# Kernel optimization log

Hardware: AMD Instinct MI355X
Metric: run time of the kernel (lower is better)

Reference implementation:

```python
import jax, jax.numpy as jnp
import numpy as np

LN_EPS = 1e-5
SUM_EPS = 1e-6
Q_EPS = 1e-8

def layernorm(x):
    # parameter-free LayerNorm over last axis (elementwise_affine=False)
    mu = jnp.mean(x, axis=-1, keepdims=True)
    var = jnp.mean(jnp.square(x - mu), axis=-1, keepdims=True)
    return (x - mu) * jax.lax.rsqrt(var + LN_EPS)

def ternary_quant(W):
    # BitNet-b1.58-style ternary quantization: scale = mean(|W|), Wq in {-1,0,1}*scale
    scale = jnp.mean(jnp.abs(W))
    Wq = jnp.clip(jnp.round(W / (scale + Q_EPS)), -1.0, 1.0) * scale
    return Wq

def setup_inputs() -> dict:
    key = jax.random.key(0)
    ks = jax.random.split(key, 8)
    B, S, F = 8, 2048, 2048
    x = jax.random.normal(ks[0], (B, S, F), dtype=jnp.float32)
    seq_pos_code = jnp.arange(S, dtype=jnp.int32)
    feature_pos_code = jnp.arange(F, dtype=jnp.int32)
    # TernaryMLP(F, F, residual=False): ternary-quantized linear F -> F
    W_v = jax.random.normal(ks[1], (F, F), dtype=jnp.float32) * (1.0 / np.sqrt(F))
    b_v = jnp.zeros((F,), dtype=jnp.float32)
    # left attn: Linear(F, 1)
    w_left = jax.random.normal(ks[2], (F, 1), dtype=jnp.float32) * (1.0 / np.sqrt(F))
    b_left = jnp.zeros((1,), dtype=jnp.float32)
    # right attn: Linear(S, 1)
    w_right = jax.random.normal(ks[3], (S, 1), dtype=jnp.float32) * (1.0 / np.sqrt(S))
    b_right = jnp.zeros((1,), dtype=jnp.float32)
    alpha = jax.random.uniform(ks[4], (1,), dtype=jnp.float32)
    return {"x": x, "seq_pos_code": seq_pos_code, "feature_pos_code": feature_pos_code,
            "W_v": W_v, "b_v": b_v, "w_left": w_left, "b_left": b_left,
            "w_right": w_right, "b_right": b_right, "alpha": alpha}

def reference(x, seq_pos_code, feature_pos_code, W_v, b_v, w_left, b_left, w_right, b_right, alpha):
    B, S, F = x.shape
    # value path: ternary-quantized linear (TernaryMLP, residual=False)
    Wq = ternary_quant(W_v)
    v = jnp.einsum('bsf,fg->bsg', x, Wq) + b_v  # [B,S,F]
    # left attention: Linear(F->1) -> [B,S,1]; transpose; LN over S; ReLU; transpose back
    la = (jnp.einsum('bsf,fo->bso', x, w_left) + b_left)[..., 0]  # [B,S]
    la = jax.nn.relu(layernorm(la))[..., None]                    # [B,S,1]
    la = la / (jnp.sum(la, axis=-1, keepdims=True) + SUM_EPS)     # normalize over last dim (size 1)
    # right attention: transpose -> [B,F,S]; Linear(S->1); transpose -> [B,1,F]; LN over F; ReLU
    ra = (jnp.einsum('bsf,so->bfo', x, w_right) + b_right)[..., 0]  # [B,F]
    ra = jax.nn.relu(layernorm(ra))[:, None, :]                     # [B,1,F]
    ra = ra / (jnp.sum(ra, axis=-1, keepdims=True) + SUM_EPS)       # normalize over F
    a = alpha[0]
    return (1.0 - a) * x + a * la * v * ra
```

## Files before the change

kernel.cpp:

```cpp
#include <hip/hip_runtime.h>
#include <hip/hip_bf16.h>
#include <stdint.h>

#define B_ 8
#define S_ 2048
#define F_ 2048
#define M_ (B_*S_)
#define K_ F_
#define N_ F_

typedef __attribute__((ext_vector_type(4))) float f32x4;
typedef __attribute__((ext_vector_type(8))) short short8;

__device__ __forceinline__ unsigned short f2bf(float f){
  unsigned u = __float_as_uint(f);
  u += 0x7FFFu + ((u >> 16) & 1u);
  return (unsigned short)(u >> 16);
}

__device__ __forceinline__ void gload16(const void* g, const void* l){
  __builtin_amdgcn_global_load_lds(
      (const __attribute__((address_space(1))) void*)g,
      (__attribute__((address_space(3))) void*)l,
      16, 0, 0);
}

__device__ __forceinline__ float waveReduce(float v){
  #pragma unroll
  for (int off = 32; off; off >>= 1) v += __shfl_down(v, off, 64);
  return v;
}

__device__ __forceinline__ float blockReduceAll(float v, float* sbuf){
  v = waveReduce(v);
  int lane = threadIdx.x & 63, w = threadIdx.x >> 6;
  __syncthreads();
  if (lane == 0) sbuf[w] = v;
  __syncthreads();
  return sbuf[0] + sbuf[1] + sbuf[2] + sbuf[3];
}

__global__ __launch_bounds__(256) void k_abs1(const float* __restrict__ W, float* __restrict__ part){
  __shared__ float sb[4];
  size_t idx = ((size_t)blockIdx.x * 256 + threadIdx.x) * 4;
  f32x4 v = *(const f32x4*)(W + idx);
  float s = fabsf(v[0]) + fabsf(v[1]) + fabsf(v[2]) + fabsf(v[3]);
  s = blockReduceAll(s, sb);
  if (threadIdx.x == 0) part[blockIdx.x] = s;
}

__global__ __launch_bounds__(256) void k_abs2(const float* __restrict__ part, float* __restrict__ scalep){
  __shared__ float sb[4];
  float s = 0.f;
  int t = threadIdx.x;
  #pragma unroll
  for (int i = 0; i < 16; i++) s += part[t + i*256];
  s = blockReduceAll(s, sb);
  if (t == 0) scalep[0] = s * (1.0f / ((float)F_ * (float)F_));
}

__global__ __launch_bounds__(256) void k_quantT(const float* __restrict__ W, unsigned short* __restrict__ BT,
                                                const float* __restrict__ scalep){
  __shared__ float tile[32][33];
  int gx = blockIdx.x * 32;
  int fy = blockIdx.y * 32;
  int tx = threadIdx.x & 31, ty = threadIdx.x >> 5;
  float inv = 1.0f / (scalep[0] + 1e-8f);
  #pragma unroll
  for (int i = 0; i < 4; i++){
    int f = fy + ty + i*8;
    tile[ty + i*8][tx] = W[(size_t)f * F_ + gx + tx];
  }
  __syncthreads();
  #pragma unroll
  for (int i = 0; i < 4; i++){
    int g = gx + ty + i*8;
    float w = tile[tx][ty + i*8];
    float t = rintf(w * inv);
    t = fminf(1.0f, fmaxf(-1.0f, t));
    BT[(size_t)g * K_ + fy + tx] = f2bf(t);
  }
}

__global__ __launch_bounds__(256) void k_front(const float* __restrict__ X, const float* __restrict__ wl,
                                               const float* __restrict__ bl, const float* __restrict__ wrt,
                                               unsigned short* __restrict__ XH, float* __restrict__ la_raw,
                                               float* __restrict__ ra_raw){
  __shared__ float lap[4][32];
  int t = threadIdx.x, w = t >> 6, lane = t & 63;
  int r0 = blockIdx.x * 32;
  int b  = r0 >> 11;
  int f0 = t * 8;
  f32x4 wl0 = *(const f32x4*)(wl + f0);
  f32x4 wl1 = *(const f32x4*)(wl + f0 + 4);
  float racc[8];
  #pragma unroll
  for (int j = 0; j < 8; j++) racc[j] = 0.f;

  for (int rr = 0; rr < 32; ++rr){
    int row = r0 + rr;
    const float* xr = X + (size_t)row * F_ + f0;
    f32x4 v0 = *(const f32x4*)(xr);
    f32x4 v1 = *(const f32x4*)(xr + 4);
    ushort4 p0, p1;
    p0.x = f2bf(v0[0]); p0.y = f2bf(v0[1]); p0.z = f2bf(v0[2]); p0.w = f2bf(v0[3]);
    p1.x = f2bf(v1[0]); p1.y = f2bf(v1[1]); p1.z = f2bf(v1[2]); p1.w = f2bf(v1[3]);
    unsigned short* xh = XH + (size_t)row * F_ + f0;
    *(ushort4*)(xh)     = p0;
    *(ushort4*)(xh + 4) = p1;
    float dot = v0[0]*wl0[0] + v0[1]*wl0[1] + v0[2]*wl0[2] + v0[3]*wl0[3]
              + v1[0]*wl1[0] + v1[1]*wl1[1] + v1[2]*wl1[2] + v1[3]*wl1[3];
    dot = waveReduce(dot);
    if (lane == 0) lap[w][rr] = dot;
    float wsr = wrt[row & (S_-1)];
    racc[0] += v0[0]*wsr; racc[1] += v0[1]*wsr; racc[2] += v0[2]*wsr; racc[3] += v0[3]*wsr;
    racc[4] += v1[0]*wsr; racc[5] += v1[1]*wsr; racc[6] += v1[2]*wsr; racc[7] += v1[3]*wsr;
  }
  __syncthreads();
  if (t < 32)
    la_raw[r0 + t] = lap[0][t] + lap[1][t] + lap[2][t] + lap[3][t] + bl[0];
  float* rb = ra_raw + b * F_ + f0;
  #pragma unroll
  for (int j = 0; j < 8; j++) atomicAdd(&rb[j], racc[j]);
}

__global__ __launch_bounds__(256) void k_ln_la(const float* __restrict__ la_raw, float* __restrict__ la){
  __shared__ float sb[4];
  int b = blockIdx.x;
  const float* p = la_raw + b * S_;
  int t = threadIdx.x;
  float v[8]; float s = 0.f, s2 = 0.f;
  #pragma unroll
  for (int i = 0; i < 8; i++){ v[i] = p[t + i*256]; s += v[i]; s2 += v[i]*v[i]; }
  s  = blockReduceAll(s,  sb);
  s2 = blockReduceAll(s2, sb);
  float mu  = s * (1.0f / S_);
  float var = s2 * (1.0f / S_) - mu*mu;
  float rstd = 1.0f / sqrtf(var + 1e-5f);
  #pragma unroll
  for (int i = 0; i < 8; i++){
    float x = (v[i] - mu) * rstd;
    x = fmaxf(x, 0.0f);
    la[b * S_ + t + i*256] = x / (x + 1e-6f);
  }
}

__global__ __launch_bounds__(256) void k_ln_ra(const float* __restrict__ ra_raw, const float* __restrict__ br,
                                               float* __restrict__ ra){
  __shared__ float sb[4];
  int b = blockIdx.x;
  const float* p = ra_raw + b * F_;
  int t = threadIdx.x;
  float bb = br[0];
  float v[8]; float s = 0.f, s2 = 0.f;
  #pragma unroll
  for (int i = 0; i < 8; i++){ v[i] = p[t + i*256] + bb; s += v[i]; s2 += v[i]*v[i]; }
  s  = blockReduceAll(s,  sb);
  s2 = blockReduceAll(s2, sb);
  float mu  = s * (1.0f / F_);
  float var = s2 * (1.0f / F_) - mu*mu;
  float rstd = 1.0f / sqrtf(var + 1e-5f);
  float r[8]; float sr = 0.f;
  #pragma unroll
  for (int i = 0; i < 8; i++){ r[i] = fmaxf((v[i] - mu) * rstd, 0.0f); sr += r[i]; }
  sr = blockReduceAll(sr, sb);
  float invs = 1.0f / (sr + 1e-6f);
  #pragma unroll
  for (int i = 0; i < 8; i++) ra[b * F_ + t + i*256] = r[i] * invs;
}

__global__ __launch_bounds__(256) void k_gemm(
    const unsigned short* __restrict__ A, const unsigned short* __restrict__ BT,
    const float* __restrict__ X, const float* __restrict__ la, const float* __restrict__ ra,
    const float* __restrict__ bv, const float* __restrict__ alphap, const float* __restrict__ scalep,
    float* __restrict__ Out)
{
  __shared__ __align__(128) char lds[32768];
  const int NBX = N_ / 128;
  int tid = threadIdx.x;
  int bid = blockIdx.x;
  const int nwg = (M_/128) * (N_/128);
  int cpx = nwg >> 3;
  int swz = (bid & 7) * cpx + (bid >> 3);
  int brow = swz / NBX, bcol = swz % NBX;
  int row0 = brow * 128, col0 = bcol * 128;

  int w = tid >> 6, lane = tid & 63;
  int wr = w >> 1, wc = w & 1;
  int lrow = lane & 15, kgrp = lane >> 4;

  f32x4 acc[4][4];
  #pragma unroll
  for (int m = 0; m < 4; m++)
    #pragma unroll
    for (int n = 0; n < 4; n++) acc[m][n] = (f32x4)(0.0f);

  int c0 = tid, c1 = tid + 256;
  int ar0 = c0 >> 2, ak0 = (((c0 & 3) ^ ((ar0 >> 1) & 3)) << 3);
  int ar1 = c1 >> 2, ak1 = (((c1 & 3) ^ ((ar1 >> 1) & 3)) << 3);
  const unsigned short* Ap0 = A  + (size_t)(row0 + ar0) * K_ + ak0;
  const unsigned short* Ap1 = A  + (size_t)(row0 + ar1) * K_ + ak1;
  const unsigned short* Bp0 = BT + (size_t)(col0 + ar0) * K_ + ak0;
  const unsigned short* Bp1 = BT + (size_t)(col0 + ar1) * K_ + ak1;
  int stoff = w * 1024;

  int aoff[4], boff[4];
  #pragma unroll
  for (int m = 0; m < 4; m++){
    int r  = wr*64 + m*16 + lrow;
    aoff[m] = r*64 + ((kgrp ^ ((r >> 1) & 3)) << 4);
    int rc = wc*64 + m*16 + lrow;
    boff[m] = 8192 + rc*64 + ((kgrp ^ ((rc >> 1) & 3)) << 4);
  }

  {
    char* base = lds;
    gload16(Ap0, base + stoff);
    gload16(Ap1, base + 4096 + stoff);
    gload16(Bp0, base + 8192 + stoff);
    gload16(Bp1, base + 12288 + stoff);
  }
  asm volatile("s_waitcnt vmcnt(0)" ::: "memory");
  __syncthreads();

  int cur = 0;
  for (int kt = 0; kt < K_/32; ++kt){
    if (kt < K_/32 - 1){
      char* nb = lds + (cur ^ 1) * 16384;
      const unsigned short* a0 = Ap0 + (kt+1)*32;
      const unsigned short* a1 = Ap1 + (kt+1)*32;
      const unsigned short* b0 = Bp0 + (kt+1)*32;
      const unsigned short* b1 = Bp1 + (kt+1)*32;
      gload16(a0, nb + stoff);
      gload16(a1, nb + 4096 + stoff);
      gload16(b0, nb + 8192 + stoff);
      gload16(b1, nb + 12288 + stoff);
    }
    const char* bb = lds + cur * 16384;
    short8 af[4], bfr[4];
    #pragma unroll
    for (int m = 0; m < 4; m++) af[m]  = *(const short8*)(bb + aoff[m]);
    #pragma unroll
    for (int n = 0; n < 4; n++) bfr[n] = *(const short8*)(bb + boff[n]);
    __builtin_amdgcn_s_setprio(1);
    #pragma unroll
    for (int m = 0; m < 4; m++)
      #pragma unroll
      for (int n = 0; n < 4; n++)
        acc[m][n] = __builtin_amdgcn_mfma_f32_16x16x32_bf16(af[m], bfr[n], acc[m][n], 0, 0, 0);
    __builtin_amdgcn_s_setprio(0);
    asm volatile("s_waitcnt vmcnt(0)" ::: "memory");
    __syncthreads();
    cur ^= 1;
  }

  float a = alphap[0];
  float scale = scalep[0];
  float oma = 1.0f - a;
  int bidx = row0 >> 11;
  const float* rab = ra + bidx * F_;
  #pragma unroll
  for (int m = 0; m < 4; m++){
    int rbase = row0 + wr*64 + m*16 + (lane >> 4) * 4;
    float lav[4];
    #pragma unroll
    for (int r = 0; r < 4; r++) lav[r] = la[rbase + r];
    #pragma unroll
    for (int n = 0; n < 4; n++){
      int col = col0 + wc*64 + n*16 + (lane & 15);
      float rav = rab[col];
      float bvv = bv[col];
      #pragma unroll
      for (int r = 0; r < 4; r++){
        int row = rbase + r;
        float v = acc[m][n][r] * scale + bvv;
        size_t idx = (size_t)row * N_ + col;
        Out[idx] = oma * X[idx] + a * lav[r] * v * rav;
      }
    }
  }
}

extern "C" void kernel_launch(void* const* d_in, const int* in_sizes, int n_in,
                              void* d_out, int out_size, void* d_ws, size_t ws_size,
                              hipStream_t stream){
  const float* x     = (const float*)d_in[0];
  const float* Wv    = (const float*)d_in[3];
  const float* bv    = (const float*)d_in[4];
  const float* wl    = (const float*)d_in[5];
  const float* bl    = (const float*)d_in[6];
  const float* wrt   = (const float*)d_in[7];
  const float* br    = (const float*)d_in[8];
  const float* alpha = (const float*)d_in[9];
  float* out = (float*)d_out;

  char* ws = (char*)d_ws;
  unsigned short* XH = (unsigned short*)(ws);
  unsigned short* BT = (unsigned short*)(ws + 67108864);
  float* la_raw = (float*)(ws + 75497472);
  float* la     = (float*)(ws + 75563008);
  float* ra_raw = (float*)(ws + 75628544);
  float* ra     = (float*)(ws + 75694080);
  float* part   = (float*)(ws + 75759616);
  float* scalep = (float*)(ws + 75776000);

  hipMemsetAsync(ra_raw, 0, B_ * F_ * sizeof(float), stream);
  k_abs1<<<4096, 256, 0, stream>>>(Wv, part);
  k_abs2<<<1, 256, 0, stream>>>(part, scalep);
  k_quantT<<<dim3(F_/32, F_/32), 256, 0, stream>>>(Wv, BT, scalep);
  k_front<<<M_/32, 256, 0, stream>>>(x, wl, bl, wrt, XH, la_raw, ra_raw);
  k_ln_la<<<B_, 256, 0, stream>>>(la_raw, la);
  k_ln_ra<<<B_, 256, 0, stream>>>(ra_raw, br, ra);
  k_gemm<<<2048, 256, 0, stream>>>(XH, BT, x, la, ra, bv, alpha, scalep, out);
}
```

Before: 527.0 us.

## Deepen GEMM LDS pipeline to four stages, merge LN kernels, unroll front loop

The GEMM main loop moves from a double-buffered LDS scheme with a full vmcnt(0) wait each step to a 4-stage ring buffer (64KB LDS), three tiles prefetched ahead and partial vmcnt waits. The aim is to hide global-to-LDS load latency behind the MFMA work. The two LayerNorm kernels become one 16-block launch, saving a launch. The front kernel processes two rows per iteration for more memory-level parallelism. The larger LDS footprint may lower occupancy per CU.

After: 465.8 us. -11.6%, faster.

```diff
diff --git a/kernel.cpp b/kernel.cpp
--- a/kernel.cpp
+++ b/kernel.cpp
@@ -97,24 +97,40 @@
   #pragma unroll
   for (int j = 0; j < 8; j++) racc[j] = 0.f;
 
-  for (int rr = 0; rr < 32; ++rr){
-    int row = r0 + rr;
-    const float* xr = X + (size_t)row * F_ + f0;
-    f32x4 v0 = *(const f32x4*)(xr);
-    f32x4 v1 = *(const f32x4*)(xr + 4);
-    ushort4 p0, p1;
-    p0.x = f2bf(v0[0]); p0.y = f2bf(v0[1]); p0.z = f2bf(v0[2]); p0.w = f2bf(v0[3]);
-    p1.x = f2bf(v1[0]); p1.y = f2bf(v1[1]); p1.z = f2bf(v1[2]); p1.w = f2bf(v1[3]);
-    unsigned short* xh = XH + (size_t)row * F_ + f0;
-    *(ushort4*)(xh)     = p0;
-    *(ushort4*)(xh + 4) = p1;
-    float dot = v0[0]*wl0[0] + v0[1]*wl0[1] + v0[2]*wl0[2] + v0[3]*wl0[3]
-              + v1[0]*wl1[0] + v1[1]*wl1[1] + v1[2]*wl1[2] + v1[3]*wl1[3];
-    dot = waveReduce(dot);
-    if (lane == 0) lap[w][rr] = dot;
-    float wsr = wrt[row & (S_-1)];
-    racc[0] += v0[0]*wsr; racc[1] += v0[1]*wsr; racc[2] += v0[2]*wsr; racc[3] += v0[3]*wsr;
-    racc[4] += v1[0]*wsr; racc[5] += v1[1]*wsr; racc[6] += v1[2]*wsr; racc[7] += v1[3]*wsr;
+  for (int rr = 0; rr < 32; rr += 2){
+    int rowA = r0 + rr, rowB = r0 + rr + 1;
+    const float* xrA = X + (size_t)rowA * F_ + f0;
+    const float* xrB = X + (size_t)rowB * F_ + f0;
+    f32x4 a0 = *(const f32x4*)(xrA);
+    f32x4 a1 = *(const f32x4*)(xrA + 4);
+    f32x4 b0 = *(const f32x4*)(xrB);
+    f32x4 b1 = *(const f32x4*)(xrB + 4);
+    ushort4 pa0, pa1, pb0, pb1;
+    pa0.x = f2bf(a0[0]); pa0.y = f2bf(a0[1]); pa0.z = f2bf(a0[2]); pa0.w = f2bf(a0[3]);
+    pa1.x = f2bf(a1[0]); pa1.y = f2bf(a1[1]); pa1.z = f2bf(a1[2]); pa1.w = f2bf(a1[3]);
+    pb0.x = f2bf(b0[0]); pb0.y = f2bf(b0[1]); pb0.z = f2bf(b0[2]); pb0.w = f2bf(b0[3]);
+    pb1.x = f2bf(b1[0]); pb1.y = f2bf(b1[1]); pb1.z = f2bf(b1[2]); pb1.w = f2bf(b1[3]);
+    unsigned short* xhA = XH + (size_t)rowA * F_ + f0;
+    unsigned short* xhB = XH + (size_t)rowB * F_ + f0;
+    *(ushort4*)(xhA)     = pa0;
+    *(ushort4*)(xhA + 4) = pa1;
+    *(ushort4*)(xhB)     = pb0;
+    *(ushort4*)(xhB + 4) = pb1;
+    float dotA = a0[0]*wl0[0] + a0[1]*wl0[1] + a0[2]*wl0[2] + a0[3]*wl0[3]
+               + a1[0]*wl1[0] + a1[1]*wl1[1] + a1[2]*wl1[2] + a1[3]*wl1[3];
+    float dotB = b0[0]*wl0[0] + b0[1]*wl0[1] + b0[2]*wl0[2] + b0[3]*wl0[3]
+               + b1[0]*wl1[0] + b1[1]*wl1[1] + b1[2]*wl1[2] + b1[3]*wl1[3];
+    #pragma unroll
+    for (int off = 32; off; off >>= 1){
+      dotA += __shfl_down(dotA, off, 64);
+      dotB += __shfl_down(dotB, off, 64);
+    }
+    if (lane == 0){ lap[w][rr] = dotA; lap[w][rr+1] = dotB; }
+    float wsA = wrt[rowA & (S_-1)], wsB = wrt[rowB & (S_-1)];
+    racc[0] += a0[0]*wsA + b0[0]*wsB; racc[1] += a0[1]*wsA + b0[1]*wsB;
+    racc[2] += a0[2]*wsA + b0[2]*wsB; racc[3] += a0[3]*wsA + b0[3]*wsB;
+    racc[4] += a1[0]*wsA + b1[0]*wsB; racc[5] += a1[1]*wsA + b1[1]*wsB;
+    racc[6] += a1[2]*wsA + b1[2]*wsB; racc[7] += a1[3]*wsA + b1[3]*wsB;
   }
   __syncthreads();
   if (t < 32)
@@ -124,49 +140,36 @@
   for (int j = 0; j < 8; j++) atomicAdd(&rb[j], racc[j]);
 }
 
-__global__ __launch_bounds__(256) void k_ln_la(const float* __restrict__ la_raw, float* __restrict__ la){
+__global__ __launch_bounds__(256) void k_ln(const float* __restrict__ la_raw, const float* __restrict__ ra_raw,
+                                            const float* __restrict__ br, float* __restrict__ la,
+                                            float* __restrict__ ra){
   __shared__ float sb[4];
-  int b = blockIdx.x;
-  const float* p = la_raw + b * S_;
+  int blk = blockIdx.x;
+  bool isRa = blk >= 8;
+  int b = blk & 7;
+  const float* p = isRa ? (ra_raw + b * F_) : (la_raw + b * S_);
   int t = threadIdx.x;
-  float v[8]; float s = 0.f, s2 = 0.f;
-  #pragma unroll
-  for (int i = 0; i < 8; i++){ v[i] = p[t + i*256]; s += v[i]; s2 += v[i]*v[i]; }
-  s  = blockReduceAll(s,  sb);
-  s2 = blockReduceAll(s2, sb);
-  float mu  = s * (1.0f / S_);
-  float var = s2 * (1.0f / S_) - mu*mu;
-  float rstd = 1.0f / sqrtf(var + 1e-5f);
-  #pragma unroll
-  for (int i = 0; i < 8; i++){
-    float x = (v[i] - mu) * rstd;
-    x = fmaxf(x, 0.0f);
-    la[b * S_ + t + i*256] = x / (x + 1e-6f);
-  }
-}
-
-__global__ __launch_bounds__(256) void k_ln_ra(const float* __restrict__ ra_raw, const float* __restrict__ br,
-                                               float* __restrict__ ra){
-  __shared__ float sb[4];
-  int b = blockIdx.x;
-  const float* p = ra_raw + b * F_;
-  int t = threadIdx.x;
-  float bb = br[0];
+  float bb = isRa ? br[0] : 0.0f;
   float v[8]; float s = 0.f, s2 = 0.f;
   #pragma unroll
   for (int i = 0; i < 8; i++){ v[i] = p[t + i*256] + bb; s += v[i]; s2 += v[i]*v[i]; }
   s  = blockReduceAll(s,  sb);
   s2 = blockReduceAll(s2, sb);
-  float mu  = s * (1.0f / F_);
-  float var = s2 * (1.0f / F_) - mu*mu;
+  float mu  = s * (1.0f / 2048.0f);
+  float var = s2 * (1.0f / 2048.0f) - mu*mu;
   float rstd = 1.0f / sqrtf(var + 1e-5f);
   float r[8]; float sr = 0.f;
   #pragma unroll
   for (int i = 0; i < 8; i++){ r[i] = fmaxf((v[i] - mu) * rstd, 0.0f); sr += r[i]; }
-  sr = blockReduceAll(sr, sb);
-  float invs = 1.0f / (sr + 1e-6f);
-  #pragma unroll
-  for (int i = 0; i < 8; i++) ra[b * F_ + t + i*256] = r[i] * invs;
+  if (isRa){
+    sr = blockReduceAll(sr, sb);
+    float invs = 1.0f / (sr + 1e-6f);
+    #pragma unroll
+    for (int i = 0; i < 8; i++) ra[b * F_ + t + i*256] = r[i] * invs;
+  } else {
+    #pragma unroll
+    for (int i = 0; i < 8; i++) la[b * S_ + t + i*256] = r[i] / (r[i] + 1e-6f);
+  }
 }
 
 __global__ __launch_bounds__(256) void k_gemm(
@@ -175,8 +178,9 @@
     const float* __restrict__ bv, const float* __restrict__ alphap, const float* __restrict__ scalep,
     float* __restrict__ Out)
 {
-  __shared__ __align__(128) char lds[32768];
+  __shared__ __align__(128) char lds[65536];
   const int NBX = N_ / 128;
+  const int NT  = K_ / 32;
   int tid = threadIdx.x;
   int bid = blockIdx.x;
   const int nwg = (M_/128) * (N_/128);
@@ -213,30 +217,21 @@
     boff[m] = 8192 + rc*64 + ((kgrp ^ ((rc >> 1) & 3)) << 4);
   }
 
-  {
-    char* base = lds;
-    gload16(Ap0, base + stoff);
-    gload16(Ap1, base + 4096 + stoff);
-    gload16(Bp0, base + 8192 + stoff);
-    gload16(Bp1, base + 12288 + stoff);
-  }
-  asm volatile("s_waitcnt vmcnt(0)" ::: "memory");
-  __syncthreads();
-
-  int cur = 0;
-  for (int kt = 0; kt < K_/32; ++kt){
-    if (kt < K_/32 - 1){
-      char* nb = lds + (cur ^ 1) * 16384;
-      const unsigned short* a0 = Ap0 + (kt+1)*32;
-      const unsigned short* a1 = Ap1 + (kt+1)*32;
-      const unsigned short* b0 = Bp0 + (kt+1)*32;
-      const unsigned short* b1 = Bp1 + (kt+1)*32;
-      gload16(a0, nb + stoff);
-      gload16(a1, nb + 4096 + stoff);
-      gload16(b0, nb + 8192 + stoff);
-      gload16(b1, nb + 12288 + stoff);
-    }
-    const char* bb = lds + cur * 16384;
+#define STAGE(T) { \
+    char* nb_ = lds + ((T) & 3) * 16384; \
+    gload16(Ap0 + (size_t)(T)*32, nb_ + stoff); \
+    gload16(Ap1 + (size_t)(T)*32, nb_ + 4096 + stoff); \
+    gload16(Bp0 + (size_t)(T)*32, nb_ + 8192 + stoff); \
+    gload16(Bp1 + (size_t)(T)*32, nb_ + 12288 + stoff); \
+  }
+
+  STAGE(0); STAGE(1); STAGE(2);
+  asm volatile("s_waitcnt vmcnt(8)" ::: "memory");
+  __builtin_amdgcn_s_barrier();
+
+  for (int kt = 0; kt < NT; ++kt){
+    if (kt + 3 < NT) STAGE(kt + 3);
+    const char* bb = lds + (kt & 3) * 16384;
     short8 af[4], bfr[4];
     #pragma unroll
     for (int m = 0; m < 4; m++) af[m]  = *(const short8*)(bb + aoff[m]);
@@ -249,10 +244,12 @@
       for (int n = 0; n < 4; n++)
         acc[m][n] = __builtin_amdgcn_mfma_f32_16x16x32_bf16(af[m], bfr[n], acc[m][n], 0, 0, 0);
     __builtin_amdgcn_s_setprio(0);
-    asm volatile("s_waitcnt vmcnt(0)" ::: "memory");
-    __syncthreads();
-    cur ^= 1;
-  }
+    if (kt + 3 < NT)      { asm volatile("s_waitcnt vmcnt(8)" ::: "memory"); }
+    else if (kt + 2 < NT) { asm volatile("s_waitcnt vmcnt(4)" ::: "memory"); }
+    else if (kt + 1 < NT) { asm volatile("s_waitcnt vmcnt(0)" ::: "memory"); }
+    if (kt + 1 < NT) __builtin_amdgcn_s_barrier();
+  }
+#undef STAGE
 
   float a = alphap[0];
   float scale = scalep[0];
@@ -309,7 +306,6 @@
   k_abs2<<<1, 256, 0, stream>>>(part, scalep);
   k_quantT<<<dim3(F_/32, F_/32), 256, 0, stream>>>(Wv, BT, scalep);
   k_front<<<M_/32, 256, 0, stream>>>(x, wl, bl, wrt, XH, la_raw, ra_raw);
-  k_ln_la<<<B_, 256, 0, stream>>>(la_raw, la);
-  k_ln_ra<<<B_, 256, 0, stream>>>(ra_raw, br, ra);
+  k_ln<<<16, 256, 0, stream>>>(la_raw, ra_raw, br, la, ra);
   k_gemm<<<2048, 256, 0, stream>>>(XH, BT, x, la, ra, bv, alpha, scalep, out);
 }
```
